# Optimization experiments

Hardware: AMD Instinct MI355X
Metric: run time of the kernel (lower is better)

Reference implementation:

```python
import jax, jax.numpy as jnp
import numpy as np

D_MODEL = 2048
N_HEADS = 16
HEAD_DIM = D_MODEL // N_HEADS
ROPE_BASE = 10000.0


def rope(x):
    # x: [b, h, s, d]; matches the torch module exactly:
    # x1 = even dims, x2 = odd dims; output = concat([x1*cos - x2*sin, x1*sin + x2*cos], -1)
    b, h, s, d = x.shape
    theta = 1.0 / ROPE_BASE ** (jnp.arange(0, d, 2, dtype=jnp.float32) / d)  # [d/2]
    angles = jnp.arange(s, dtype=jnp.float32)[:, None] * theta[None, :]       # [s, d/2]
    cos = jnp.cos(angles)[None, None]  # [1,1,s,d/2]
    sin = jnp.sin(angles)[None, None]
    x1, x2 = x[..., ::2], x[..., 1::2]
    return jnp.concatenate([x1 * cos - x2 * sin, x1 * sin + x2 * cos], axis=-1)


def setup_inputs() -> dict:
    key = jax.random.key(0)
    ks = jax.random.split(key, 5)
    b, s = 2, 2048
    x = jax.random.normal(ks[0], (b, s, D_MODEL), dtype=jnp.float32)
    scale_in = 1.0 / np.sqrt(D_MODEL)
    Wqkv = jax.random.normal(ks[1], (D_MODEL, 3 * D_MODEL), dtype=jnp.float32) * scale_in
    bqkv = jnp.zeros((3 * D_MODEL,), dtype=jnp.float32)
    Wo = jax.random.normal(ks[2], (D_MODEL, D_MODEL), dtype=jnp.float32) * scale_in
    bo = jnp.zeros((D_MODEL,), dtype=jnp.float32)
    return {"x": x, "Wqkv": Wqkv, "bqkv": bqkv, "Wo": Wo, "bo": bo}


def reference(x, Wqkv, bqkv, Wo, bo):
    b, s, d = x.shape
    qkv = x @ Wqkv + bqkv                      # [b, s, 3d]
    q, k, v = jnp.split(qkv, 3, axis=-1)
    def to_heads(t):
        return t.reshape(b, s, N_HEADS, HEAD_DIM).transpose(0, 2, 1, 3)  # [b,h,s,hd]
    q, k, v = to_heads(q), to_heads(k), to_heads(v)
    q = rope(q)
    k = rope(k)
    scores = jnp.einsum('bhqd,bhkd->bhqk', q, k) / jnp.sqrt(jnp.float32(HEAD_DIM))
    attn = jax.nn.softmax(scores, axis=-1)
    out = jnp.einsum('bhqk,bhkd->bhqd', attn, v)
    out = out.transpose(0, 2, 1, 3).reshape(b, s, d)
    return out @ Wo + bo
```

## Files before the change

### kernel.cpp

```cpp
#include <hip/hip_runtime.h>
#include <hip/hip_bf16.h>
#include <cstdint>
#include <type_traits>

#define D_MODEL 2048
#define NH 16
#define HD 128
#define SEQ 2048
#define QKV_LD (3 * D_MODEL)

typedef __attribute__((ext_vector_type(8))) short short8;
typedef __attribute__((ext_vector_type(4))) float f32x4;
typedef __attribute__((ext_vector_type(16))) float f32x16;

__device__ __forceinline__ ushort f2bf(float f) {
    union { float f; uint32_t u; } c; c.f = f;
    uint32_t u = c.u;
    uint32_t r = (u + 0x7FFFu + ((u >> 16) & 1u)) >> 16;
    return (ushort)r;
}
__device__ __forceinline__ float bf2f(ushort b) {
    union { uint32_t u; float f; } c; c.u = ((uint32_t)b) << 16;
    return c.f;
}

__device__ __forceinline__ void load_lds16(const ushort* g, ushort* l) {
    __builtin_amdgcn_global_load_lds(
        (const __attribute__((address_space(1))) void*)g,
        (__attribute__((address_space(3))) void*)l, 16, 0, 0);
}

#define WAITV(N) asm volatile("s_waitcnt vmcnt(" #N ")" ::: "memory")
#define BARF()   do { __builtin_amdgcn_s_barrier(); \
                      asm volatile("" ::: "memory"); } while (0)
#define PRIO1    __builtin_amdgcn_s_setprio(1)
#define PRIO0    __builtin_amdgcn_s_setprio(0)

__device__ __forceinline__ void transpose_body(const float* __restrict__ in,
                                               ushort* __restrict__ out,
                                               int R, int C, int bx, int by, int t,
                                               float (*tile)[33]) {
    int tx = t & 31, ty = t >> 5;
    int c0 = bx * 32, r0 = by * 32;
    for (int i = 0; i < 4; ++i) {
        int r = r0 + ty + i * 8;
        tile[ty + i * 8][tx] = in[(size_t)r * C + c0 + tx];
    }
    __syncthreads();
    for (int i = 0; i < 4; ++i) {
        int c = c0 + ty + i * 8;
        out[(size_t)c * R + r0 + tx] = f2bf(tile[tx][ty + i * 8]);
    }
}

__global__ void prep_fused(const float* __restrict__ x, ushort* __restrict__ x_bf,
                           const float* __restrict__ Wqkv, ushort* __restrict__ wqkvT,
                           const float* __restrict__ Wo, ushort* __restrict__ woT,
                           float2* __restrict__ rtab) {
    __shared__ float tile[32][33];
    int blk = blockIdx.x;
    int t = threadIdx.x;
    if (blk < 512) {
        int i = blk * 256 + t;
        int s = i >> 6, j = i & 63;
        float theta = powf(10000.0f, -(float)j * (1.0f / 64.0f));
        float ang = (float)s * theta;
        float sn, cs;
        sincosf(ang, &sn, &cs);
        rtab[i] = make_float2(cs, sn);
    } else if (blk < 8704) {
        int idx = (blk - 512) * 256 + t;
        float4 v = ((const float4*)x)[idx];
        ushort4 o;
        o.x = f2bf(v.x); o.y = f2bf(v.y); o.z = f2bf(v.z); o.w = f2bf(v.w);
        ((ushort4*)x_bf)[idx] = o;
    } else if (blk < 20992) {
        int i = blk - 8704;
        transpose_body(Wqkv, wqkvT, 2048, 6144, i % 192, i / 192, t, tile);
    } else {
        int i = blk - 20992;
        transpose_body(Wo, woT, 2048, 2048, i & 63, i >> 6, t, tile);
    }
}

#define B_ROWOFF(L) (NHALF == 2 ? (((L) & 1) * 128 + ((L) >> 1) * 32) : ((L) * 64))
#define STAGE_A(L, T_, B_) load_lds16(Ag + (size_t)(L) * 64 * K + (size_t)(T_) * 64, \
                                      smA + (B_) * 16384 + (L) * 4096 + ldsW)
#define STAGE_B(L, T_, B_) load_lds16(Bg + (size_t)B_ROWOFF(L) * K + (size_t)(T_) * 64, \
                                      smB + (B_) * (8192 * NHALF) + (L) * 4096 + ldsW)
#define READ_A(MH) do { const ushort* _ab = smA + cb * 16384 + aRow + (MH) * 4096; \
    _Pragma("unroll") for (int i_ = 0; i_ < 4; ++i_) { \
        af[i_][0] = *(const short8*)(_ab + i_ * 1024 + pc0); \
        af[i_][1] = *(const short8*)(_ab + i_ * 1024 + pc1); } } while (0)
#define READ_BH(dst, NHh) do { const ushort* _bb = smB + cb * (8192 * NHALF) + (NHh) * 8192 + bRow; \
    _Pragma("unroll") for (int j_ = 0; j_ < 2; ++j_) { \
        dst[j_][0] = *(const short8*)(_bb + j_ * 1024 + pc0); \
        dst[j_][1] = *(const short8*)(_bb + j_ * 1024 + pc1); } } while (0)
#define MFMA_PH(MH, NHh, bf) do { \
    _Pragma("unroll") for (int i_ = 0; i_ < 4; ++i_) \
    _Pragma("unroll") for (int j_ = 0; j_ < 2; ++j_) { \
        acc[(MH) * 4 + i_][(NHh) * 2 + j_] = __builtin_amdgcn_mfma_f32_16x16x32_bf16( \
            af[i_][0], bf[j_][0], acc[(MH) * 4 + i_][(NHh) * 2 + j_], 0, 0, 0); \
        acc[(MH) * 4 + i_][(NHh) * 2 + j_] = __builtin_amdgcn_mfma_f32_16x16x32_bf16( \
            af[i_][1], bf[j_][1], acc[(MH) * 4 + i_][(NHh) * 2 + j_], 0, 0, 0); } } while (0)

template <typename OutT, int NHALF>
__global__ __launch_bounds__(512, 2) void gemm256(
    const ushort* __restrict__ A,
    const ushort* __restrict__ Bt,
    const float* __restrict__ bias,
    OutT* __restrict__ C,
    int M, int N, int K)
{
    __shared__ __align__(16) ushort sm[32768 + 2 * 8192 * NHALF];
    ushort* smA = sm;
    ushort* smB = sm + 32768;

    int t = threadIdx.x;
    int w = t >> 6, lane = t & 63;
    int lr = lane & 15, lh = lane >> 4;
    int wm_idx = w >> 2, wn_idx = w & 3;
    int m0 = blockIdx.y * 256, n0 = blockIdx.x * (128 * NHALF);

    int srow = t >> 3;
    int scol = ((t & 7) ^ (srow & 7)) << 3;
    const ushort* Ag = A + (size_t)(m0 + srow) * K + scol;
    int bq = (NHALF == 2) ? ((srow >> 5) * 64 + (srow & 31)) : srow;
    const ushort* Bg = Bt + (size_t)(n0 + bq) * K + scol;
    int ldsW = w * 512;

    int pc0 = (lh ^ (lr & 7)) << 3;
    int pc1 = ((4 + lh) ^ (lr & 7)) << 3;
    int aRow = (wm_idx * 128 + lr) * 64;
    int bRow = (wn_idx * 32 + lr) * 64;

    f32x4 acc[8][2 * NHALF];
#pragma unroll
    for (int i = 0; i < 8; ++i)
#pragma unroll
        for (int j = 0; j < 2 * NHALF; ++j) acc[i][j] = (f32x4)0.0f;
    short8 af[4][2], bf0[2][2], bf1[2][2];

    int NT = K >> 6;

    if constexpr (NHALF == 2) {
        STAGE_A(0, 0, 0); STAGE_A(2, 0, 0); STAGE_B(0, 0, 0); STAGE_B(1, 0, 0);
        STAGE_B(2, 0, 0); STAGE_B(3, 0, 0);
        STAGE_A(1, 0, 0); STAGE_A(3, 0, 0);
        WAITV(4);
    } else {
        STAGE_A(0, 0, 0); STAGE_A(2, 0, 0); STAGE_B(0, 0, 0);
        STAGE_B(1, 0, 0); STAGE_A(1, 0, 0); STAGE_A(3, 0, 0);
        WAITV(2);
    }
    BARF();

    for (int T = 0; T < NT; ++T) {
        int cb = T & 1, nb = cb ^ 1;
        bool pf = (T + 1 < NT);
        if constexpr (NHALF == 2) {
            READ_A(0); READ_BH(bf0, 0);
            if (pf) { STAGE_A(0, T + 1, nb); STAGE_A(2, T + 1, nb);
                      STAGE_B(0, T + 1, nb); STAGE_B(1, T + 1, nb); }
            BARF();
            PRIO1; MFMA_PH(0, 0, bf0); PRIO0;
            if (pf) WAITV(6); else WAITV(2);
            BARF();
            READ_BH(bf1, 1);
            if (pf) { STAGE_B(2, T + 1, nb); STAGE_B(3, T + 1, nb); }
            BARF();
            PRIO1; MFMA_PH(0, 1, bf1); PRIO0;
            if (pf) WAITV(6); else WAITV(0);
            BARF();
            READ_A(1);
            if (pf) { STAGE_A(1, T + 1, nb); STAGE_A(3, T + 1, nb); }
            BARF();
            PRIO1; MFMA_PH(1, 1, bf1); MFMA_PH(1, 0, bf0); PRIO0;
            if (pf) WAITV(4);
            BARF();
        } else {
            READ_A(0); READ_BH(bf0, 0);
            if (pf) { STAGE_A(0, T + 1, nb); STAGE_A(2, T + 1, nb); STAGE_B(0, T + 1, nb); }
            BARF();
            PRIO1; MFMA_PH(0, 0, bf0); PRIO0;
            if (pf) WAITV(3); else WAITV(0);
            BARF();
            READ_A(1);
            if (pf) { STAGE_B(1, T + 1, nb); STAGE_A(1, T + 1, nb); STAGE_A(3, T + 1, nb); }
            BARF();
            PRIO1; MFMA_PH(1, 0, bf0); PRIO0;
            if (pf) WAITV(2);
            BARF();
        }
    }

    float bv[2 * NHALF];
#pragma unroll
    for (int jj = 0; jj < 2 * NHALF; ++jj) bv[jj] = bias[n0 + wn_idx * 32 * NHALF + jj * 16 + lr];
#pragma unroll
    for (int ii = 0; ii < 8; ++ii) {
        int row = m0 + wm_idx * 128 + ii * 16 + lh * 4;
#pragma unroll
        for (int jj = 0; jj < 2 * NHALF; ++jj) {
            int col = n0 + wn_idx * 32 * NHALF + jj * 16 + lr;
#pragma unroll
            for (int r = 0; r < 4; ++r) {
                float v = acc[ii][jj][r] + bv[jj];
                if constexpr (std::is_same<OutT, ushort>::value)
                    C[(size_t)(row + r) * N + col] = f2bf(v);
                else
                    C[(size_t)(row + r) * N + col] = v;
            }
        }
    }
}

#define STAGE_A3(L, T_, B_) load_lds16(Ag + (size_t)(L) * 64 * K + (size_t)(T_) * 64, \
                                       smA + (B_) * 8192 + (L) * 4096 + ldsW)
#define STAGE_B3(L, T_, B_) load_lds16(Bg + (size_t)((((L) & 1) * 2 + wnp) * 96 + ((L) >> 1) * 32 + rb) * K + (size_t)(T_) * 64, \
                                       smB + (B_) * 24576 + (L) * 4096 + ldsW)
#define READ_A3() do { const ushort* _ab = smA + cb * 8192 + aRow; \
    _Pragma("unroll") for (int i_ = 0; i_ < 4; ++i_) { \
        af[i_][0] = *(const short8*)(_ab + i_ * 1024 + pc0); \
        af[i_][1] = *(const short8*)(_ab + i_ * 1024 + pc1); } } while (0)
#define READ_B3(H) do { const ushort* _bb = smB + cb * 24576 + (H) * 8192 + bRow; \
    _Pragma("unroll") for (int j_ = 0; j_ < 2; ++j_) { \
        bfr[j_][0] = *(const short8*)(_bb + j_ * 1024 + pc0); \
        bfr[j_][1] = *(const short8*)(_bb + j_ * 1024 + pc1); } } while (0)
#define MFMA_P3(H) do { \
    _Pragma("unroll") for (int i_ = 0; i_ < 4; ++i_) \
    _Pragma("unroll") for (int j_ = 0; j_ < 2; ++j_) { \
        acc[i_][(H) * 2 + j_] = __builtin_amdgcn_mfma_f32_16x16x32_bf16( \
            af[i_][0], bfr[j_][0], acc[i_][(H) * 2 + j_], 0, 0, 0); \
        acc[i_][(H) * 2 + j_] = __builtin_amdgcn_mfma_f32_16x16x32_bf16( \
            af[i_][1], bfr[j_][1], acc[i_][(H) * 2 + j_], 0, 0, 0); } } while (0)

__global__ __launch_bounds__(512, 2) void gemm384(
    const ushort* __restrict__ A,
    const ushort* __restrict__ Bt,
    const float* __restrict__ bias,
    ushort* __restrict__ C,
    int M, int N, int K)
{
    __shared__ __align__(16) ushort sm[65536];
    ushort* smA = sm;
    ushort* smB = sm + 16384;

    int t = threadIdx.x;
    int w = t >> 6, lane = t & 63;
    int lr = lane & 15, lh = lane >> 4;
    int wm_idx = w >> 2, wn_idx = w & 3;
    int m0 = blockIdx.y * 128, n0 = blockIdx.x * 384;

    int srow = t >> 3;
    int scol = ((t & 7) ^ (srow & 7)) << 3;
    const ushort* Ag = A + (size_t)(m0 + srow) * K + scol;
    const ushort* Bg = Bt + (size_t)n0 * K + scol;
    int wnp = srow >> 5;
    int rb = srow & 31;
    int ldsW = w * 512;

    int pc0 = (lh ^ (lr & 7)) << 3;
    int pc1 = ((4 + lh) ^ (lr & 7)) << 3;
    int aRow = (wm_idx * 64 + lr) * 64;
    int bRow = (wn_idx * 32 + lr) * 64;

    f32x4 acc[4][6];
#pragma unroll
    for (int i = 0; i < 4; ++i)
#pragma unroll
        for (int j = 0; j < 6; ++j) acc[i][j] = (f32x4)0.0f;
    short8 af[4][2], bfr[2][2];

    int NT = K >> 6;

    STAGE_A3(0, 0, 0); STAGE_A3(1, 0, 0); STAGE_B3(0, 0, 0); STAGE_B3(1, 0, 0);
    STAGE_B3(2, 0, 0); STAGE_B3(3, 0, 0); STAGE_B3(4, 0, 0); STAGE_B3(5, 0, 0);
    WAITV(4);
    BARF();

    for (int T = 0; T < NT; ++T) {
        int cb = T & 1, nb = cb ^ 1;
        bool pf = (T + 1 < NT);
        READ_A3(); READ_B3(0);
        if (pf) { STAGE_A3(0, T + 1, nb); STAGE_A3(1, T + 1, nb); STAGE_B3(0, T + 1, nb); }
        BARF();
        PRIO1; MFMA_P3(0); PRIO0;
        if (pf) WAITV(5); else WAITV(2);
        BARF();
        READ_B3(1);
        if (pf) { STAGE_B3(1, T + 1, nb); STAGE_B3(2, T + 1, nb); STAGE_B3(3, T + 1, nb); }
        BARF();
        PRIO1; MFMA_P3(1); PRIO0;
        if (pf) WAITV(6); else WAITV(0);
        BARF();
        READ_B3(2);
        if (pf) { STAGE_B3(4, T + 1, nb); STAGE_B3(5, T + 1, nb); }
        BARF();
        PRIO1; MFMA_P3(2); PRIO0;
        if (pf) WAITV(4);
        BARF();
    }

    float bv[6];
#pragma unroll
    for (int jj = 0; jj < 6; ++jj) bv[jj] = bias[n0 + wn_idx * 96 + jj * 16 + lr];
#pragma unroll
    for (int ii = 0; ii < 4; ++ii) {
        int row = m0 + wm_idx * 64 + ii * 16 + lh * 4;
#pragma unroll
        for (int jj = 0; jj < 6; ++jj) {
            int col = n0 + wn_idx * 96 + jj * 16 + lr;
#pragma unroll
            for (int r = 0; r < 4; ++r) {
                float v = acc[ii][jj][r] + bv[jj];
                C[(size_t)(row + r) * N + col] = f2bf(v);
            }
        }
    }
}

__global__ void rope_v_fused(const ushort* __restrict__ qkv, const float2* __restrict__ tab,
                             ushort* __restrict__ Qb, ushort* __restrict__ Kb,
                             ushort* __restrict__ Vt) {
    __shared__ ushort tile[32][33];
    int blk = blockIdx.x;
    int t = threadIdx.x;
    if (blk < 32768) {
        int wv = blk * 4 + (t >> 6);
        int j = t & 63;
        int bs = wv >> 5;
        int rem = wv & 31;
        int which = rem >> 4;
        int h = rem & 15;
        int s = bs & 2047;
        int b = bs >> 11;
        size_t src = (size_t)bs * QKV_LD + which * D_MODEL + h * HD;
        uint32_t pr = *(const uint32_t*)(qkv + src + 2 * j);
        float x1 = bf2f((ushort)(pr & 0xffff));
        float x2 = bf2f((ushort)(pr >> 16));
        float2 cspair = tab[(s << 6) + j];
        float cs = cspair.x, sn = cspair.y;
        float sc = which ? 1.0f : 0.08838834764831845f;
        float o1 = (x1 * cs - x2 * sn) * sc;
        float o2 = (x1 * sn + x2 * cs) * sc;
        ushort* dst = which ? Kb : Qb;
        size_t obase = ((size_t)(b * NH + h) * SEQ + s) * HD;
        dst[obase + j] = f2bf(o1);
        dst[obase + 64 + j] = f2bf(o2);
    } else {
        int i = blk - 32768;
        int bx = i & 63, by = (i >> 6) & 3, bz = i >> 8;
        int tx = t & 31, ty = t >> 5;
        int s0 = bx * 32;
        int d0 = by * 32;
        int bh = bz;
        int b = bh >> 4, h = bh & 15;
        for (int k = 0; k < 4; ++k) {
            int s = s0 + ty + k * 8;
            tile[ty + k * 8][tx] = qkv[((size_t)(b * SEQ + s)) * QKV_LD + 2 * D_MODEL + h * HD + d0 + tx];
        }
        __syncthreads();
        for (int k = 0; k < 4; ++k) {
            int d = d0 + ty + k * 8;
            Vt[((size_t)bh * HD + d) * SEQ + s0 + tx] = tile[tx][ty + k * 8];
        }
    }
}

__global__ __launch_bounds__(256) void attn_mfma(const ushort* __restrict__ Qb,
                                                 const ushort* __restrict__ Kb,
                                                 const ushort* __restrict__ Vt,
                                                 ushort* __restrict__ ctx) {
    __shared__ ushort smem[25600];
    ushort* Ks = smem;
    ushort* Vts = smem + 8192;
    ushort* Ps = smem + 16384;

    int t = threadIdx.x;
    int w = t >> 6, l = t & 63;
    int l31 = l & 31, g = l >> 5;
    int flat = blockIdx.y * 16 + blockIdx.x;
    int wid = (flat & 7) * 64 + (flat >> 3);
    int q0 = (wid & 15) * 128;
    int bh = wid >> 4;
    int b = bh >> 4, h = bh & 15;

    int qrow = q0 + w * 32 + l31;
    const ushort* Qg = Qb + ((size_t)bh * SEQ + qrow) * HD;
    short8 qf[8];
#pragma unroll
    for (int kc = 0; kc < 8; kc++)
        qf[kc] = *(const short8*)(Qg + kc * 16 + g * 8);

    f32x16 O[4];
#pragma unroll
    for (int di = 0; di < 4; di++) O[di] = (f32x16)0.0f;
    float m_run = -INFINITY, l_run = 0.0f;

    const ushort* KgB = Kb + (size_t)bh * SEQ * HD;
    const ushort* VtB = Vt + (size_t)bh * HD * SEQ;

    for (int k0 = 0; k0 < SEQ; k0 += 64) {
        __syncthreads();
#pragma unroll
        for (int c2 = 0; c2 < 4; c2++) {
            int f = c2 * 256 + t;
            int r = f >> 4, c = f & 15;
            int cp = c ^ (r & 15);
            uint4 v = *(const uint4*)(KgB + (size_t)(k0 + r) * HD + c * 8);
            *(uint4*)(Ks + r * 128 + cp * 8) = v;
        }
#pragma unroll
        for (int c2 = 0; c2 < 4; c2++) {
            int f = c2 * 256 + t;
            int d = f >> 3, c = f & 7;
            int cp = c ^ (d & 7);
            uint4 v = *(const uint4*)(VtB + (size_t)d * SEQ + k0 + c * 8);
            *(uint4*)(Vts + d * 64 + cp * 8) = v;
        }
        __syncthreads();

        f32x16 St[2];
        St[0] = (f32x16)0.0f;
        St[1] = (f32x16)0.0f;
#pragma unroll
        for (int ki = 0; ki < 2; ki++) {
            int row = ki * 32 + l31;
#pragma unroll
            for (int kc = 0; kc < 8; kc++) {
                int cp = (kc * 2 + g) ^ (row & 15);
                short8 a = *(const short8*)(Ks + row * 128 + cp * 8);
                St[ki] = __builtin_amdgcn_mfma_f32_32x32x16_bf16(a, qf[kc], St[ki], 0, 0, 0);
            }
        }

        float mx = -INFINITY;
#pragma unroll
        for (int ki = 0; ki < 2; ki++)
#pragma unroll
            for (int r = 0; r < 16; r++) mx = fmaxf(mx, St[ki][r]);
        mx = fmaxf(mx, __shfl_xor(mx, 32));
        float mn = fmaxf(m_run, mx);
        float alpha = __expf(m_run - mn);
        m_run = mn;
        float psum = 0.0f;
#pragma unroll
        for (int ki = 0; ki < 2; ki++)
#pragma unroll
            for (int r = 0; r < 16; r++) {
                float p = __expf(St[ki][r] - mn);
                St[ki][r] = p;
                psum += p;
            }
        psum += __shfl_xor(psum, 32);
        l_run = l_run * alpha + psum;
#pragma unroll
        for (int di = 0; di < 4; di++)
#pragma unroll
            for (int r = 0; r < 16; r++) O[di][r] *= alpha;

        {
            int qloc = w * 32 + l31;
            ushort* Pr = Ps + qloc * 72;
#pragma unroll
            for (int ki = 0; ki < 2; ki++)
#pragma unroll
                for (int u = 0; u < 4; u++) {
                    ushort4 pk;
                    pk.x = f2bf(St[ki][4 * u + 0]);
                    pk.y = f2bf(St[ki][4 * u + 1]);
                    pk.z = f2bf(St[ki][4 * u + 2]);
                    pk.w = f2bf(St[ki][4 * u + 3]);
                    *(ushort4*)(Pr + ki * 32 + 8 * u + 4 * g) = pk;
                }
        }

        {
            int qloc = w * 32 + l31;
            short8 pb[4];
#pragma unroll
            for (int kc = 0; kc < 4; kc++)
                pb[kc] = *(const short8*)(Ps + qloc * 72 + kc * 16 + g * 8);
#pragma unroll
            for (int di = 0; di < 4; di++) {
                int d = di * 32 + l31;
#pragma unroll
                for (int kc = 0; kc < 4; kc++) {
                    int cp = (kc * 2 + g) ^ (d & 7);
                    short8 va = *(const short8*)(Vts + d * 64 + cp * 8);
                    O[di] = __builtin_amdgcn_mfma_f32_32x32x16_bf16(va, pb[kc], O[di], 0, 0, 0);
                }
            }
        }
    }

    __syncthreads();
    float inv = 1.0f / l_run;
    ushort* ob = smem;
    {
        int qloc = w * 32 + l31;
        ushort* orow = ob + qloc * 128;
#pragma unroll
        for (int di = 0; di < 4; di++)
#pragma unroll
            for (int u = 0; u < 4; u++) {
                ushort4 pk;
                pk.x = f2bf(O[di][4 * u + 0] * inv);
                pk.y = f2bf(O[di][4 * u + 1] * inv);
                pk.z = f2bf(O[di][4 * u + 2] * inv);
                pk.w = f2bf(O[di][4 * u + 3] * inv);
                *(ushort4*)(orow + di * 32 + 8 * u + 4 * g) = pk;
            }
    }
#pragma unroll
    for (int p = 0; p < 8; p++) {
        int qloc = w * 32 + p * 4 + (l >> 4);
        int c16 = l & 15;
        uint4 v = *(const uint4*)(ob + qloc * 128 + c16 * 8);
        size_t tok = (size_t)b * SEQ + q0 + qloc;
        *(uint4*)(ctx + tok * D_MODEL + h * HD + c16 * 8) = v;
    }
}

extern "C" void kernel_launch(void* const* d_in, const int* in_sizes, int n_in,
                              void* d_out, int out_size, void* d_ws, size_t ws_size,
                              hipStream_t stream) {
    const float* x    = (const float*)d_in[0];
    const float* Wqkv = (const float*)d_in[1];
    const float* bqkv = (const float*)d_in[2];
    const float* Wo   = (const float*)d_in[3];
    const float* bo   = (const float*)d_in[4];
    float* out = (float*)d_out;

    char* ws = (char*)d_ws;
    ushort* x_bf   = (ushort*)(ws);
    ushort* wqkvT  = (ushort*)(ws + 16777216);
    ushort* woT    = (ushort*)(ws + 41943040);
    ushort* qkv_bf = (ushort*)(ws + 50331648);
    ushort* Qb     = (ushort*)(ws + 100663296);
    ushort* Kb     = (ushort*)(ws + 117440512);
    ushort* VtG    = (ushort*)(ws + 134217728);
    ushort* ctx    = (ushort*)(ws + 150994944);
    float2* rtab   = (float2*)(ws + 150994944);

    prep_fused<<<25088, 256, 0, stream>>>(x, x_bf, Wqkv, wqkvT, Wo, woT, rtab);
    gemm384<<<dim3(16, 32), 512, 0, stream>>>(x_bf, wqkvT, bqkv, qkv_bf, 4096, 6144, 2048);
    rope_v_fused<<<40960, 256, 0, stream>>>(qkv_bf, rtab, Qb, Kb, VtG);
    attn_mfma<<<dim3(16, 32), 256, 0, stream>>>(Qb, Kb, VtG, ctx);
    gemm256<float, 1><<<dim3(16, 16), 512, 0, stream>>>(ctx, woT, bo, out, 4096, 2048, 2048);
}
```

Measured before the change: 408.2 us.

## Keep P in registers via lane shuffles and add lazy softmax rescaling

The attention kernel no longer writes the bf16 probability tile to LDS and reads it back as the MFMA B operand. Each lane instead packs pairs of floats with bf16x2 conversion and exchanges half its values with the partner lane 32 away through shuffles, building the operand in registers. This removes an LDS round trip and shrinks shared memory, which could allow higher occupancy. It also skips the running-max update and the rescale of O unless some lane's max grows by more than 8, which saves exp and multiply work but lets unnormalised values grow up to e^8 before rescaling.

```diff
diff --git a/kernel.cpp b/kernel.cpp
--- a/kernel.cpp
+++ b/kernel.cpp
@@ -372,14 +372,14 @@
                                                  const ushort* __restrict__ Kb,
                                                  const ushort* __restrict__ Vt,
                                                  ushort* __restrict__ ctx) {
-    __shared__ ushort smem[25600];
+    __shared__ ushort smem[16384];
     ushort* Ks = smem;
     ushort* Vts = smem + 8192;
-    ushort* Ps = smem + 16384;
 
     int t = threadIdx.x;
     int w = t >> 6, l = t & 63;
     int l31 = l & 31, g = l >> 5;
+    bool gb = (g != 0);
     int flat = blockIdx.y * 16 + blockIdx.x;
     int wid = (flat & 7) * 64 + (flat >> 3);
     int q0 = (wid & 15) * 128;
@@ -441,56 +441,60 @@
 #pragma unroll
             for (int r = 0; r < 16; r++) mx = fmaxf(mx, St[ki][r]);
         mx = fmaxf(mx, __shfl_xor(mx, 32));
-        float mn = fmaxf(m_run, mx);
-        float alpha = __expf(m_run - mn);
-        m_run = mn;
+        if (!__all(mx - m_run <= 8.0f)) {
+            float mn = fmaxf(m_run, mx);
+            float alpha = __expf(m_run - mn);
+            m_run = mn;
+            l_run *= alpha;
+#pragma unroll
+            for (int di = 0; di < 4; di++)
+#pragma unroll
+                for (int r = 0; r < 16; r++) O[di][r] *= alpha;
+        }
         float psum = 0.0f;
 #pragma unroll
         for (int ki = 0; ki < 2; ki++)
 #pragma unroll
             for (int r = 0; r < 16; r++) {
-                float p = __expf(St[ki][r] - mn);
+                float p = __expf(St[ki][r] - m_run);
                 St[ki][r] = p;
                 psum += p;
             }
         psum += __shfl_xor(psum, 32);
-        l_run = l_run * alpha + psum;
-#pragma unroll
-        for (int di = 0; di < 4; di++)
-#pragma unroll
-            for (int r = 0; r < 16; r++) O[di][r] *= alpha;
-
-        {
-            int qloc = w * 32 + l31;
-            ushort* Pr = Ps + qloc * 72;
-#pragma unroll
-            for (int ki = 0; ki < 2; ki++)
-#pragma unroll
-                for (int u = 0; u < 4; u++) {
-                    ushort4 pk;
-                    pk.x = f2bf(St[ki][4 * u + 0]);
-                    pk.y = f2bf(St[ki][4 * u + 1]);
-                    pk.z = f2bf(St[ki][4 * u + 2]);
-                    pk.w = f2bf(St[ki][4 * u + 3]);
-                    *(ushort4*)(Pr + ki * 32 + 8 * u + 4 * g) = pk;
-                }
-        }
-
-        {
-            int qloc = w * 32 + l31;
-            short8 pb[4];
-#pragma unroll
-            for (int kc = 0; kc < 4; kc++)
-                pb[kc] = *(const short8*)(Ps + qloc * 72 + kc * 16 + g * 8);
-#pragma unroll
-            for (int di = 0; di < 4; di++) {
-                int d = di * 32 + l31;
-#pragma unroll
-                for (int kc = 0; kc < 4; kc++) {
-                    int cp = (kc * 2 + g) ^ (d & 7);
-                    short8 va = *(const short8*)(Vts + d * 64 + cp * 8);
-                    O[di] = __builtin_amdgcn_mfma_f32_32x32x16_bf16(va, pb[kc], O[di], 0, 0, 0);
-                }
+        l_run += psum;
+
+        short8 pb[4];
+#pragma unroll
+        for (int kc = 0; kc < 4; kc++) {
+            int ki = kc >> 1;
+            int base = (kc & 1) * 8;
+            union { __hip_bfloat162 b; uint32_t u; } c00, c01, c10, c11;
+            c00.b = __float22bfloat162_rn(make_float2(St[ki][base + 0], St[ki][base + 1]));
+            c01.b = __float22bfloat162_rn(make_float2(St[ki][base + 2], St[ki][base + 3]));
+            c10.b = __float22bfloat162_rn(make_float2(St[ki][base + 4], St[ki][base + 5]));
+            c11.b = __float22bfloat162_rn(make_float2(St[ki][base + 6], St[ki][base + 7]));
+            uint32_t sA = gb ? c10.u : c00.u;
+            uint32_t sB = gb ? c11.u : c01.u;
+            uint32_t sC = gb ? c00.u : c10.u;
+            uint32_t sD = gb ? c01.u : c11.u;
+            uint32_t oC = (uint32_t)__shfl_xor((int)sC, 32);
+            uint32_t oD = (uint32_t)__shfl_xor((int)sD, 32);
+            union { uint32_t wdo[4]; short8 s; } u;
+            u.wdo[0] = gb ? oC : sA;
+            u.wdo[1] = gb ? oD : sB;
+            u.wdo[2] = gb ? sA : oC;
+            u.wdo[3] = gb ? sB : oD;
+            pb[kc] = u.s;
+        }
+
+#pragma unroll
+        for (int di = 0; di < 4; di++) {
+            int d = di * 32 + l31;
+#pragma unroll
+            for (int kc = 0; kc < 4; kc++) {
+                int cp = (kc * 2 + g) ^ (d & 7);
+                short8 va = *(const short8*)(Vts + d * 64 + cp * 8);
+                O[di] = __builtin_amdgcn_mfma_f32_32x32x16_bf16(va, pb[kc], O[di], 0, 0, 0);
             }
         }
     }
```

Result: slower. 433.4 us (+6.2%).

## Prefetch next K/V tile into registers and skip softmax rescale when max stable

Applied to the files above, without the earlier changes.

The attention loop now loads the next 64-key K and V^T tiles into registers right after the LDS barrier, so the global loads overlap with the QK^T MFMA and softmax work of the current tile. The register copies are then stored to shared memory at the top of the next iteration. Separately, the running-max update and the rescale of O and l are skipped when no lane's new max exceeds the running max by more than 8, a lazy-rescaling trick. This adds register pressure from the eight uint4 prefetch registers, and the exp values are then bounded by e^8 rather than 1, which could cost some bf16 precision in P.

```diff
diff --git a/kernel.cpp b/kernel.cpp
--- a/kernel.cpp
+++ b/kernel.cpp
@@ -401,25 +401,36 @@
     const ushort* KgB = Kb + (size_t)bh * SEQ * HD;
     const ushort* VtB = Vt + (size_t)bh * HD * SEQ;
 
+    uint4 kreg[4], vreg[4];
+#define ISSUE_KV(K0_) do { \
+    _Pragma("unroll") for (int c2_ = 0; c2_ < 4; c2_++) { \
+        int f_ = c2_ * 256 + t; \
+        int r_ = f_ >> 4, ck_ = f_ & 15; \
+        kreg[c2_] = *(const uint4*)(KgB + (size_t)((K0_) + r_) * HD + ck_ * 8); \
+        int d_ = f_ >> 3, cv_ = f_ & 7; \
+        vreg[c2_] = *(const uint4*)(VtB + (size_t)d_ * SEQ + (K0_) + cv_ * 8); \
+    } } while (0)
+
+    ISSUE_KV(0);
+
     for (int k0 = 0; k0 < SEQ; k0 += 64) {
         __syncthreads();
+        WAITV(0);
 #pragma unroll
         for (int c2 = 0; c2 < 4; c2++) {
             int f = c2 * 256 + t;
             int r = f >> 4, c = f & 15;
             int cp = c ^ (r & 15);
-            uint4 v = *(const uint4*)(KgB + (size_t)(k0 + r) * HD + c * 8);
-            *(uint4*)(Ks + r * 128 + cp * 8) = v;
-        }
-#pragma unroll
-        for (int c2 = 0; c2 < 4; c2++) {
-            int f = c2 * 256 + t;
-            int d = f >> 3, c = f & 7;
-            int cp = c ^ (d & 7);
-            uint4 v = *(const uint4*)(VtB + (size_t)d * SEQ + k0 + c * 8);
-            *(uint4*)(Vts + d * 64 + cp * 8) = v;
+            *(uint4*)(Ks + r * 128 + cp * 8) = kreg[c2];
+            int d = f >> 3, c7 = f & 7;
+            int cpv = c7 ^ (d & 7);
+            *(uint4*)(Vts + d * 64 + cpv * 8) = vreg[c2];
         }
         __syncthreads();
+        if (k0 + 64 < SEQ) {
+            ISSUE_KV(k0 + 64);
+            asm volatile("" ::: "memory");
+        }
 
         f32x16 St[2];
         St[0] = (f32x16)0.0f;
@@ -441,24 +452,27 @@
 #pragma unroll
             for (int r = 0; r < 16; r++) mx = fmaxf(mx, St[ki][r]);
         mx = fmaxf(mx, __shfl_xor(mx, 32));
-        float mn = fmaxf(m_run, mx);
-        float alpha = __expf(m_run - mn);
-        m_run = mn;
+        if (!__all(mx - m_run <= 8.0f)) {
+            float mn = fmaxf(m_run, mx);
+            float alpha = __expf(m_run - mn);
+            m_run = mn;
+            l_run *= alpha;
+#pragma unroll
+            for (int di = 0; di < 4; di++)
+#pragma unroll
+                for (int r = 0; r < 16; r++) O[di][r] *= alpha;
+        }
         float psum = 0.0f;
 #pragma unroll
         for (int ki = 0; ki < 2; ki++)
 #pragma unroll
             for (int r = 0; r < 16; r++) {
-                float p = __expf(St[ki][r] - mn);
+                float p = __expf(St[ki][r] - m_run);
                 St[ki][r] = p;
                 psum += p;
             }
         psum += __shfl_xor(psum, 32);
-        l_run = l_run * alpha + psum;
-#pragma unroll
-        for (int di = 0; di < 4; di++)
-#pragma unroll
-            for (int r = 0; r < 16; r++) O[di][r] *= alpha;
+        l_run += psum;
 
         {
             int qloc = w * 32 + l31;
```

Result: slower. 523.1 us (+28.2%).
